# Kernel optimization log

Measured on AMD Instinct MI355X. Metric: run time of the kernel, lower is better.

Reference implementation:

```python
import jax, jax.numpy as jnp
import numpy as np

DIM = 384
HEADS = 6
HIDDEN = int(DIM * 4.0)
EPS = 1e-6

def setup_inputs() -> dict:
    key = jax.random.key(0)
    ks = jax.random.split(key, 8)
    s = 0.02
    return {
        "x": jax.random.normal(ks[0], (4, 2048, DIM), dtype=jnp.float32),
        "w_qkv": jax.random.normal(ks[1], (DIM, 3 * DIM), dtype=jnp.float32) * s,
        "b_qkv": jnp.zeros((3 * DIM,), dtype=jnp.float32),
        "w_proj": jax.random.normal(ks[2], (DIM, DIM), dtype=jnp.float32) * s,
        "b_proj": jnp.zeros((DIM,), dtype=jnp.float32),
        "w_fc1": jax.random.normal(ks[3], (DIM, HIDDEN), dtype=jnp.float32) * s,
        "b_fc1": jnp.zeros((HIDDEN,), dtype=jnp.float32),
        "w_fc2": jax.random.normal(ks[4], (HIDDEN, DIM), dtype=jnp.float32) * s,
        "b_fc2": jnp.zeros((DIM,), dtype=jnp.float32),
        "g1": jnp.ones((DIM,), dtype=jnp.float32),
        "beta1": jnp.zeros((DIM,), dtype=jnp.float32),
        "g2": jnp.ones((DIM,), dtype=jnp.float32),
        "beta2": jnp.zeros((DIM,), dtype=jnp.float32),
    }

def _layernorm(x, g, b):
    mu = jnp.mean(x, axis=-1, keepdims=True)
    var = jnp.mean(jnp.square(x - mu), axis=-1, keepdims=True)
    return (x - mu) * jax.lax.rsqrt(var + EPS) * g + b

def _attention(x, w_qkv, b_qkv, w_proj, b_proj):
    B, N, C = x.shape
    H = HEADS
    Dh = C // H
    qkv = x @ w_qkv + b_qkv                      # [B,N,3C]
    qkv = qkv.reshape(B, N, 3, H, Dh)
    q = jnp.transpose(qkv[:, :, 0], (0, 2, 1, 3))  # [B,H,N,Dh]
    k = jnp.transpose(qkv[:, :, 1], (0, 2, 1, 3))
    v = jnp.transpose(qkv[:, :, 2], (0, 2, 1, 3))
    scale = Dh ** -0.5
    attn = jnp.einsum('bhnd,bhmd->bhnm', q, k) * scale
    attn = jax.nn.softmax(attn, axis=-1)
    out = jnp.einsum('bhnm,bhmd->bhnd', attn, v)
    out = jnp.transpose(out, (0, 2, 1, 3)).reshape(B, N, C)
    return out @ w_proj + b_proj

def _mlp(x, w_fc1, b_fc1, w_fc2, b_fc2):
    h = jax.nn.gelu(x @ w_fc1 + b_fc1, approximate=False)
    return h @ w_fc2 + b_fc2

def reference(x, w_qkv, b_qkv, w_proj, b_proj, w_fc1, b_fc1, w_fc2, b_fc2, g1, beta1, g2, beta2):
    x = x + _attention(_layernorm(x, g1, beta1), w_qkv, b_qkv, w_proj, b_proj)
    x = x + _mlp(_layernorm(x, g2, beta2), w_fc1, b_fc1, w_fc2, b_fc2)
    return x
```

## Files before the change

### kernel.cpp

```cpp
#include <hip/hip_runtime.h>
#include <hip/hip_bf16.h>

#define TOK 8192
#define CDIM 384
#define HEADS 6
#define DH 64
#define HID 1536
#define SEQ 2048

#define QSCALE 0.18033688011112042f

typedef short bf16x8 __attribute__((ext_vector_type(8)));
typedef short bf16x4 __attribute__((ext_vector_type(4)));
typedef float f32x4 __attribute__((ext_vector_type(4)));
typedef float f32x16 __attribute__((ext_vector_type(16)));
typedef void __attribute__((address_space(1))) GV;
typedef void __attribute__((address_space(3))) SV;

__device__ __forceinline__ short f2bf(float f) {
    __hip_bfloat16 h = __float2bfloat16(f);
    return *reinterpret_cast<short*>(&h);
}

__device__ __forceinline__ int pack_bf2(float a, float b) {
    __hip_bfloat162 h2 = __float22bfloat162_rn(make_float2(a, b));
    int r;
    __builtin_memcpy(&r, &h2, 4);
    return r;
}

__device__ __forceinline__ void gl_lds16(const short* g, short* lds) {
    __builtin_amdgcn_global_load_lds((GV*)g, (SV*)lds, 16, 0, 0);
}

__device__ __forceinline__ float gelu_fast(float v) {
    const float A = 2.3022067f;
    const float B = 0.1029442f;
    const float u = v * (A + B * v * v);
    return v - v / (1.0f + exp2f(u));
}

__global__ __launch_bounds__(128) void ln_trans(const float* __restrict__ x,
                                                const float* __restrict__ g,
                                                const float* __restrict__ bta,
                                                short* __restrict__ y,
                                                const float* __restrict__ w_qkv,
                                                const float* __restrict__ w_proj,
                                                const float* __restrict__ w_fc1,
                                                const float* __restrict__ w_fc2,
                                                short* __restrict__ qkvT,
                                                short* __restrict__ projT,
                                                short* __restrict__ fc1T,
                                                short* __restrict__ fc2T) {
    if (blockIdx.x < TOK) {
        const int row = blockIdx.x;
        const float* xr = x + (size_t)row * CDIM;
        const int t = threadIdx.x;
        float v0 = xr[t], v1 = xr[t + 128], v2 = xr[t + 256];
        float s = v0 + v1 + v2;
        float ss = v0 * v0 + v1 * v1 + v2 * v2;
#pragma unroll
        for (int off = 1; off < 64; off <<= 1) {
            s += __shfl_xor(s, off);
            ss += __shfl_xor(ss, off);
        }
        __shared__ float sh[4];
        const int wv = t >> 6;
        if ((t & 63) == 0) { sh[wv] = s; sh[2 + wv] = ss; }
        __syncthreads();
        s = sh[0] + sh[1];
        ss = sh[2] + sh[3];
        const float mu = s * (1.0f / CDIM);
        const float var = ss * (1.0f / CDIM) - mu * mu;
        const float rs = rsqrtf(var + 1e-6f);
        short* yr = y + (size_t)row * CDIM;
        yr[t]       = f2bf((v0 - mu) * rs * g[t]       + bta[t]);
        yr[t + 128] = f2bf((v1 - mu) * rs * g[t + 128] + bta[t + 128]);
        yr[t + 256] = f2bf((v2 - mu) * rs * g[t + 256] + bta[t + 256]);
        return;
    }
    int b = blockIdx.x - TOK;
    const float* w; short* o; int K, N, nb;
    if (b < 432)       { w = w_qkv;  o = qkvT;  K = 384;  N = 1152; nb = 36; }
    else if (b < 576)  { b -= 432;  w = w_proj; o = projT; K = 384;  N = 384;  nb = 12; }
    else if (b < 1152) { b -= 576;  w = w_fc1;  o = fc1T;  K = 384;  N = 1536; nb = 48; }
    else               { b -= 1152; w = w_fc2;  o = fc2T;  K = 1536; N = 384;  nb = 12; }
    const int bx = (b % nb) * 32, by = (b / nb) * 32;
    __shared__ float t[32][33];
    const int tx = threadIdx.x & 31, ty = threadIdx.x >> 5;
#pragma unroll
    for (int i = 0; i < 8; ++i)
        t[ty + i * 4][tx] = w[(size_t)(by + ty + i * 4) * N + bx + tx];
    __syncthreads();
#pragma unroll
    for (int i = 0; i < 8; ++i)
        o[(size_t)(bx + ty + i * 4) * K + by + tx] = f2bf(t[tx][ty + i * 4]);
}

__global__ __launch_bounds__(128) void ln_kernel(const float* __restrict__ x,
                                                 const float* __restrict__ g,
                                                 const float* __restrict__ bta,
                                                 short* __restrict__ y) {
    const int row = blockIdx.x;
    const float* xr = x + (size_t)row * CDIM;
    const int t = threadIdx.x;
    float v0 = xr[t], v1 = xr[t + 128], v2 = xr[t + 256];
    float s = v0 + v1 + v2;
    float ss = v0 * v0 + v1 * v1 + v2 * v2;
#pragma unroll
    for (int off = 1; off < 64; off <<= 1) {
        s += __shfl_xor(s, off);
        ss += __shfl_xor(ss, off);
    }
    __shared__ float sh[4];
    const int wv = t >> 6;
    if ((t & 63) == 0) { sh[wv] = s; sh[2 + wv] = ss; }
    __syncthreads();
    s = sh[0] + sh[1];
    ss = sh[2] + sh[3];
    const float mu = s * (1.0f / CDIM);
    const float var = ss * (1.0f / CDIM) - mu * mu;
    const float rs = rsqrtf(var + 1e-6f);
    short* yr = y + (size_t)row * CDIM;
    yr[t]       = f2bf((v0 - mu) * rs * g[t]       + bta[t]);
    yr[t + 128] = f2bf((v1 - mu) * rs * g[t + 128] + bta[t + 128]);
    yr[t + 256] = f2bf((v2 - mu) * rs * g[t + 256] + bta[t + 256]);
}

template <int MODE, int MT>
__global__ __launch_bounds__(256) void mfma_gemm(const short* __restrict__ A,
                                                 const short* __restrict__ WT,
                                                 const float* __restrict__ bias,
                                                 const float* __restrict__ resid,
                                                 float* __restrict__ outF,
                                                 short* __restrict__ outB,
                                                 short* __restrict__ qb,
                                                 short* __restrict__ kb,
                                                 short* __restrict__ vtb,
                                                 int M, int N, int K) {
    constexpr int BN = (MT == 4) ? 128 : 64;
    constexpr int BM = (MT == 1) ? 64 : 128;
    __shared__ __align__(16) short As[BM * 64];
    __shared__ __align__(16) short Bs[BN * 64];

    const int tid  = threadIdx.x;
    const int w    = tid >> 6;
    const int lane = tid & 63;
    const int quad = lane >> 4;
    const int n15  = lane & 15;
    const int wr   = (MT == 4) ? (w >> 1) : w;
    const int wc   = (MT == 4) ? (w & 1) : 0;
    const int m0   = blockIdx.y * BM;
    const int n0   = blockIdx.x * BN;
    const int swz  = n15 & 7;

    f32x4 acc[MT][4];
#pragma unroll
    for (int i = 0; i < MT; ++i)
#pragma unroll
        for (int j = 0; j < 4; ++j) {
            acc[i][j][0] = 0; acc[i][j][1] = 0; acc[i][j][2] = 0; acc[i][j][3] = 0;
        }

    for (int k0 = 0; k0 < K; k0 += 64) {
        __syncthreads();
#pragma unroll
        for (int i = 0; i < BM / 32; ++i) {
            const int c = i * 256 + tid;
            const int r = c >> 3, p = c & 7;
            gl_lds16(A + (size_t)(m0 + r) * K + k0 + ((p ^ (r & 7)) * 8),
                     As + (i * 256 + w * 64) * 8);
        }
#pragma unroll
        for (int i = 0; i < BN / 32; ++i) {
            const int c = i * 256 + tid;
            const int r = c >> 3, p = c & 7;
            gl_lds16(WT + (size_t)(n0 + r) * K + k0 + ((p ^ (r & 7)) * 8),
                     Bs + (i * 256 + w * 64) * 8);
        }
        __syncthreads();

#pragma unroll
        for (int kk = 0; kk < 2; ++kk) {
            bf16x8 af[MT], bfr[4];
#pragma unroll
            for (int mt = 0; mt < MT; ++mt)
                af[mt] = *(const bf16x8*)&As[(wr * (MT * 16) + mt * 16 + n15) * 64 +
                                             (((kk * 4 + quad) ^ swz) * 8)];
#pragma unroll
            for (int nt = 0; nt < 4; ++nt)
                bfr[nt] = *(const bf16x8*)&Bs[(wc * 64 + nt * 16 + n15) * 64 +
                                              (((kk * 4 + quad) ^ swz) * 8)];
#pragma unroll
            for (int mt = 0; mt < MT; ++mt)
#pragma unroll
                for (int nt = 0; nt < 4; ++nt)
                    acc[mt][nt] = __builtin_amdgcn_mfma_f32_16x16x32_bf16(af[mt], bfr[nt], acc[mt][nt], 0, 0, 0);
        }
    }

#pragma unroll
    for (int nt = 0; nt < 4; ++nt) {
        const int col = n0 + wc * 64 + nt * 16 + n15;
        const float bv = bias[col];
        if constexpr (MODE == 2) {
            const int part = col / CDIM;
            const int rem  = col - part * CDIM;
            const int h    = rem >> 6;
            const int d    = rem & 63;
#pragma unroll
            for (int mt = 0; mt < MT; ++mt) {
                const int r0 = m0 + wr * (MT * 16) + mt * 16 + quad * 4;
                const int bi = r0 >> 11;
                const int n  = r0 & 2047;
                if (part == 2) {
                    short4 pkv;
                    pkv.x = f2bf(acc[mt][nt][0] + bv);
                    pkv.y = f2bf(acc[mt][nt][1] + bv);
                    pkv.z = f2bf(acc[mt][nt][2] + bv);
                    pkv.w = f2bf(acc[mt][nt][3] + bv);
                    *(short4*)&vtb[((size_t)(bi * HEADS + h) * DH + d) * SEQ + n] = pkv;
                } else {
                    short* dst = (part == 0 ? qb : kb) +
                                 ((size_t)(bi * HEADS + h) * SEQ + n) * DH + d;
#pragma unroll
                    for (int rr = 0; rr < 4; ++rr) {
                        float o = acc[mt][nt][rr] + bv;
                        if (part == 0) o *= QSCALE;
                        dst[(size_t)rr * DH] = f2bf(o);
                    }
                }
            }
        } else {
#pragma unroll
            for (int mt = 0; mt < MT; ++mt)
#pragma unroll
                for (int rr = 0; rr < 4; ++rr) {
                    const int r = m0 + wr * (MT * 16) + mt * 16 + quad * 4 + rr;
                    float o = acc[mt][nt][rr] + bv;
                    if constexpr (MODE == 1) {
                        outB[(size_t)r * N + col] = f2bf(gelu_fast(o));
                    } else {
                        if (resid) o += resid[(size_t)r * N + col];
                        outF[(size_t)r * N + col] = o;
                    }
                }
        }
    }
}

__global__ __launch_bounds__(256, 4) void attn_mfma(const short* __restrict__ qb,
                                                    const short* __restrict__ kb,
                                                    const short* __restrict__ vtb,
                                                    short* __restrict__ outp) {
    __shared__ __align__(16) char smem[33792];

    const int bid = blockIdx.x;
    const int x   = bid & 7;
    const int j   = bid >> 3;
    const int bh  = x * 3 + (j >> 6);
    const int qt  = j & 63;
    const int bi  = bh / HEADS;
    const int h   = bh - bi * HEADS;

    const int tid  = threadIdx.x;
    const int w    = tid >> 6;
    const int lane = tid & 63;
    const int l31  = lane & 31;
    const int hi   = lane >> 5;

    short* Kl  = (short*)(smem + w * 8192);
    short* Vtl = (short*)(smem + w * 8192 + 4096);

    const size_t headoff = (size_t)bh * SEQ * DH;

    bf16x8 qf[4];
    {
        const short* qg = qb + headoff + (size_t)(qt * 32 + l31) * DH + hi * 8;
#pragma unroll
        for (int kc = 0; kc < 4; ++kc)
            qf[kc] = *(const bf16x8*)(qg + kc * 16);
    }

    const int l3 = lane >> 3, l7 = lane & 7;
    const int l2 = lane >> 2, p4 = lane & 3;
    const short* kg = kb + headoff + (size_t)(w * 32 + l3) * DH + ((l7 ^ l3) * 8);
    const short* vg = vtb + (size_t)bh * DH * SEQ + (size_t)l2 * SEQ +
                      ((p4 ^ (l2 & 3)) * 8) + w * 32;

    const int swk = l31 & 7;
    const int swv = l31 & 3;
    const int krd = l31 * 64;
    const int vrd = l31 * 32;

    f32x16 O0 = {}, O1 = {};
    float lp = 0.0f;
    const f32x16 Zc = {};

    for (int t = 0; t < SEQ / 128; ++t) {
#pragma unroll
        for (int i = 0; i < 4; ++i) {
            gl_lds16(kg + i * 512, Kl + i * 512);
            gl_lds16(vg + (size_t)i * 16 * SEQ, Vtl + i * 512);
        }
        kg += 128 * DH;
        vg += 128;
        asm volatile("s_waitcnt vmcnt(0)" ::: "memory");
        __builtin_amdgcn_wave_barrier();

        bf16x8 kf0 = *(const bf16x8*)&Kl[krd + (((0 + hi) ^ swk) * 8)];
        bf16x8 kf1 = *(const bf16x8*)&Kl[krd + (((2 + hi) ^ swk) * 8)];
        bf16x8 kf2 = *(const bf16x8*)&Kl[krd + (((4 + hi) ^ swk) * 8)];
        bf16x8 kf3 = *(const bf16x8*)&Kl[krd + (((6 + hi) ^ swk) * 8)];

        f32x16 S = __builtin_amdgcn_mfma_f32_32x32x16_bf16(kf0, qf[0], Zc, 0, 0, 0);
        S = __builtin_amdgcn_mfma_f32_32x32x16_bf16(kf1, qf[1], S, 0, 0, 0);
        S = __builtin_amdgcn_mfma_f32_32x32x16_bf16(kf2, qf[2], S, 0, 0, 0);
        S = __builtin_amdgcn_mfma_f32_32x32x16_bf16(kf3, qf[3], S, 0, 0, 0);

        bf16x8 v00 = *(const bf16x8*)&Vtl[vrd + ((hi ^ swv) * 8)];
        bf16x8 v01 = *(const bf16x8*)&Vtl[vrd + (((2 + hi) ^ swv) * 8)];
        bf16x8 v10 = *(const bf16x8*)&Vtl[1024 + vrd + ((hi ^ swv) * 8)];
        bf16x8 v11 = *(const bf16x8*)&Vtl[1024 + vrd + (((2 + hi) ^ swv) * 8)];

        float e[16];
#pragma unroll
        for (int r = 0; r < 16; ++r) e[r] = exp2f(S[r]);
        lp += (((e[0] + e[1]) + (e[2] + e[3])) + ((e[4] + e[5]) + (e[6] + e[7]))) +
              (((e[8] + e[9]) + (e[10] + e[11])) + ((e[12] + e[13]) + (e[14] + e[15])));

        int p0 = pack_bf2(e[0], e[1]),  p1 = pack_bf2(e[2], e[3]);
        int p2 = pack_bf2(e[4], e[5]),  p3 = pack_bf2(e[6], e[7]);
        asm("v_permlane32_swap_b32 %0, %1" : "+v"(p0), "+v"(p2));
        asm("v_permlane32_swap_b32 %0, %1" : "+v"(p1), "+v"(p3));
        int p4w = pack_bf2(e[8], e[9]),  p5 = pack_bf2(e[10], e[11]);
        int p6 = pack_bf2(e[12], e[13]), p7 = pack_bf2(e[14], e[15]);
        asm("v_permlane32_swap_b32 %0, %1" : "+v"(p4w), "+v"(p6));
        asm("v_permlane32_swap_b32 %0, %1" : "+v"(p5), "+v"(p7));
        bf16x8 pf0, pf1;
        { int pw[4] = {p0, p1, p2, p3};   __builtin_memcpy(&pf0, pw, 16); }
        { int pw[4] = {p4w, p5, p6, p7};  __builtin_memcpy(&pf1, pw, 16); }

        O0 = __builtin_amdgcn_mfma_f32_32x32x16_bf16(v00, pf0, O0, 0, 0, 0);
        O0 = __builtin_amdgcn_mfma_f32_32x32x16_bf16(v01, pf1, O0, 0, 0, 0);
        O1 = __builtin_amdgcn_mfma_f32_32x32x16_bf16(v10, pf0, O1, 0, 0, 0);
        O1 = __builtin_amdgcn_mfma_f32_32x32x16_bf16(v11, pf1, O1, 0, 0, 0);
    }

    lp += __shfl_xor(lp, 32);

    __syncthreads();
    float* Obuf = (float*)smem;
    float* lbuf = (float*)(smem + 33280);
    float* myO  = Obuf + w * 2080;
#pragma unroll
    for (int r = 0; r < 16; ++r) {
        const int d0 = (r & 3) + 8 * (r >> 2) + 4 * hi;
        myO[l31 * 65 + d0]      = O0[r];
        myO[l31 * 65 + 32 + d0] = O1[r];
    }
    if (hi == 0) lbuf[w * 32 + l31] = lp;
    __syncthreads();

    const int quad = lane >> 4;
    const int n15  = lane & 15;
    const int d = w * 16 + n15;
#pragma unroll
    for (int i = 0; i < 8; ++i) {
        const int q = quad * 8 + i;
        const float l = lbuf[q] + lbuf[32 + q] + lbuf[64 + q] + lbuf[96 + q];
        const float s = Obuf[q * 65 + d] + Obuf[2080 + q * 65 + d] +
                        Obuf[4160 + q * 65 + d] + Obuf[6240 + q * 65 + d];
        outp[(size_t)(bi * SEQ + qt * 32 + q) * CDIM + h * DH + d] = f2bf(s / l);
    }
}

extern "C" void kernel_launch(void* const* d_in, const int* in_sizes, int n_in,
                              void* d_out, int out_size, void* d_ws, size_t ws_size,
                              hipStream_t stream) {
    const float* x      = (const float*)d_in[0];
    const float* w_qkv  = (const float*)d_in[1];
    const float* b_qkv  = (const float*)d_in[2];
    const float* w_proj = (const float*)d_in[3];
    const float* b_proj = (const float*)d_in[4];
    const float* w_fc1  = (const float*)d_in[5];
    const float* b_fc1  = (const float*)d_in[6];
    const float* w_fc2  = (const float*)d_in[7];
    const float* b_fc2  = (const float*)d_in[8];
    const float* g1     = (const float*)d_in[9];
    const float* beta1  = (const float*)d_in[10];
    const float* g2     = (const float*)d_in[11];
    const float* beta2  = (const float*)d_in[12];
    float* out = (float*)d_out;

    short* qkvT = (short*)d_ws;
    short* projT = qkvT + 1152 * 384;
    short* fc1T  = projT + 384 * 384;
    short* fc2T  = fc1T + 1536 * 384;
    short* y     = fc2T + 384 * 1536;
    short* qb    = y + (size_t)TOK * 384;
    short* kb    = qb + (size_t)TOK * 384;
    short* vtb   = kb + (size_t)TOK * 384;
    short* attn  = vtb + (size_t)TOK * 384;
    short* hbuf  = attn + (size_t)TOK * 384;

    ln_trans<<<TOK + 1728, 128, 0, stream>>>(x, g1, beta1, y,
                                             w_qkv, w_proj, w_fc1, w_fc2,
                                             qkvT, projT, fc1T, fc2T);
    mfma_gemm<2, 4><<<dim3(1152 / 128, TOK / 128), 256, 0, stream>>>(
        y, qkvT, b_qkv, nullptr, nullptr, nullptr, qb, kb, vtb, TOK, 3 * CDIM, CDIM);
    attn_mfma<<<1536, 256, 0, stream>>>(qb, kb, vtb, attn);
    mfma_gemm<0, 1><<<dim3(CDIM / 64, TOK / 64), 256, 0, stream>>>(
        attn, projT, b_proj, x, out, nullptr, nullptr, nullptr, nullptr, TOK, CDIM, CDIM);
    ln_kernel<<<TOK, 128, 0, stream>>>(out, g2, beta2, y);
    mfma_gemm<1, 4><<<dim3(HID / 128, TOK / 128), 256, 0, stream>>>(
        y, fc1T, b_fc1, nullptr, nullptr, hbuf, nullptr, nullptr, nullptr, TOK, HID, CDIM);
    mfma_gemm<0, 1><<<dim3(CDIM / 64, TOK / 64), 256, 0, stream>>>(
        hbuf, fc2T, b_fc2, out, out, nullptr, nullptr, nullptr, nullptr, TOK, CDIM, HID);
}
```

Baseline: 236.0 us.

## Prefetch next K/V tile during compute and compute row sums via MFMA

The attention inner loop now issues the next iteration's K loads right after the current K fragments are read into registers, and likewise for V. Fine-grained vmcnt waits let global-to-LDS copies overlap the QK and PV matrix multiplies, where before every iteration stalled on a full wait. The softmax row sum is now accumulated with an extra MFMA against a vector of bf16 ones, replacing the scalar adds and the final shuffle. This adds two MFMAs per iteration and sums the bf16-rounded probabilities rather than the fp32 values. Correctness relies on the single per-wave LDS buffer being refilled only after its fragments have been read.

New measurement: 235.0 us. About the same (-0.4%).

```diff
diff --git a/kernel.cpp b/kernel.cpp
--- a/kernel.cpp
+++ b/kernel.cpp
@@ -281,6 +281,7 @@
         for (int kc = 0; kc < 4; ++kc)
             qf[kc] = *(const bf16x8*)(qg + kc * 16);
     }
+    asm volatile("s_waitcnt vmcnt(0)" ::: "memory");
 
     const int l3 = lane >> 3, l7 = lane & 7;
     const int l2 = lane >> 2, p4 = lane & 3;
@@ -293,41 +294,61 @@
     const int krd = l31 * 64;
     const int vrd = l31 * 32;
 
-    f32x16 O0 = {}, O1 = {};
-    float lp = 0.0f;
+    f32x16 O0 = {}, O1 = {}, Lc = {};
     const f32x16 Zc = {};
 
+    bf16x8 ones;
+    {
+        const short one = 0x3F80;
+#pragma unroll
+        for (int i = 0; i < 8; ++i) ones[i] = one;
+    }
+
+#define STAGE_K(tt) { const short* kgt = kg + (size_t)(tt) * 128 * DH;             \
+        _Pragma("unroll") for (int i = 0; i < 4; ++i)                              \
+            gl_lds16(kgt + i * 512, Kl + i * 512); }
+#define STAGE_V(tt) { const short* vgt = vg + (tt) * 128;                          \
+        _Pragma("unroll") for (int i = 0; i < 4; ++i)                              \
+            gl_lds16(vgt + (size_t)i * 16 * SEQ, Vtl + i * 512); }
+
+    STAGE_K(0);
+    STAGE_V(0);
+
     for (int t = 0; t < SEQ / 128; ++t) {
-#pragma unroll
-        for (int i = 0; i < 4; ++i) {
-            gl_lds16(kg + i * 512, Kl + i * 512);
-            gl_lds16(vg + (size_t)i * 16 * SEQ, Vtl + i * 512);
-        }
-        kg += 128 * DH;
-        vg += 128;
-        asm volatile("s_waitcnt vmcnt(0)" ::: "memory");
-        __builtin_amdgcn_wave_barrier();
+        asm volatile("s_waitcnt vmcnt(4)" ::: "memory");
+        __builtin_amdgcn_sched_barrier(0);
 
         bf16x8 kf0 = *(const bf16x8*)&Kl[krd + (((0 + hi) ^ swk) * 8)];
         bf16x8 kf1 = *(const bf16x8*)&Kl[krd + (((2 + hi) ^ swk) * 8)];
         bf16x8 kf2 = *(const bf16x8*)&Kl[krd + (((4 + hi) ^ swk) * 8)];
         bf16x8 kf3 = *(const bf16x8*)&Kl[krd + (((6 + hi) ^ swk) * 8)];
+        asm volatile("s_waitcnt lgkmcnt(0)" ::: "memory");
+        __builtin_amdgcn_sched_barrier(0);
+        if (t < SEQ / 128 - 1) STAGE_K(t + 1);
 
         f32x16 S = __builtin_amdgcn_mfma_f32_32x32x16_bf16(kf0, qf[0], Zc, 0, 0, 0);
         S = __builtin_amdgcn_mfma_f32_32x32x16_bf16(kf1, qf[1], S, 0, 0, 0);
         S = __builtin_amdgcn_mfma_f32_32x32x16_bf16(kf2, qf[2], S, 0, 0, 0);
         S = __builtin_amdgcn_mfma_f32_32x32x16_bf16(kf3, qf[3], S, 0, 0, 0);
 
+        if (t < SEQ / 128 - 1) {
+            asm volatile("s_waitcnt vmcnt(4)" ::: "memory");
+        } else {
+            asm volatile("s_waitcnt vmcnt(0)" ::: "memory");
+        }
+        __builtin_amdgcn_sched_barrier(0);
+
         bf16x8 v00 = *(const bf16x8*)&Vtl[vrd + ((hi ^ swv) * 8)];
         bf16x8 v01 = *(const bf16x8*)&Vtl[vrd + (((2 + hi) ^ swv) * 8)];
         bf16x8 v10 = *(const bf16x8*)&Vtl[1024 + vrd + ((hi ^ swv) * 8)];
         bf16x8 v11 = *(const bf16x8*)&Vtl[1024 + vrd + (((2 + hi) ^ swv) * 8)];
+        asm volatile("s_waitcnt lgkmcnt(0)" ::: "memory");
+        __builtin_amdgcn_sched_barrier(0);
+        if (t < SEQ / 128 - 1) STAGE_V(t + 1);
 
         float e[16];
 #pragma unroll
         for (int r = 0; r < 16; ++r) e[r] = exp2f(S[r]);
-        lp += (((e[0] + e[1]) + (e[2] + e[3])) + ((e[4] + e[5]) + (e[6] + e[7]))) +
-              (((e[8] + e[9]) + (e[10] + e[11])) + ((e[12] + e[13]) + (e[14] + e[15])));
 
         int p0 = pack_bf2(e[0], e[1]),  p1 = pack_bf2(e[2], e[3]);
         int p2 = pack_bf2(e[4], e[5]),  p3 = pack_bf2(e[6], e[7]);
@@ -345,9 +366,11 @@
         O0 = __builtin_amdgcn_mfma_f32_32x32x16_bf16(v01, pf1, O0, 0, 0, 0);
         O1 = __builtin_amdgcn_mfma_f32_32x32x16_bf16(v10, pf0, O1, 0, 0, 0);
         O1 = __builtin_amdgcn_mfma_f32_32x32x16_bf16(v11, pf1, O1, 0, 0, 0);
-    }
-
-    lp += __shfl_xor(lp, 32);
+        Lc = __builtin_amdgcn_mfma_f32_32x32x16_bf16(ones, pf0, Lc, 0, 0, 0);
+        Lc = __builtin_amdgcn_mfma_f32_32x32x16_bf16(ones, pf1, Lc, 0, 0, 0);
+    }
+#undef STAGE_K
+#undef STAGE_V
 
     __syncthreads();
     float* Obuf = (float*)smem;
@@ -359,7 +382,7 @@
         myO[l31 * 65 + d0]      = O0[r];
         myO[l31 * 65 + 32 + d0] = O1[r];
     }
-    if (hi == 0) lbuf[w * 32 + l31] = lp;
+    if (hi == 0) lbuf[w * 32 + l31] = Lc[0];
     __syncthreads();
 
     const int quad = lane >> 4;
```
